# Kernel optimization log

Measured on AMD Instinct MI355X. Metric: run time of the kernel, lower is better.

Reference implementation:

```python
import jax, jax.numpy as jnp
import numpy as np

P_DROP = 0.1

def setup_inputs() -> dict:
    key = jax.random.key(0)
    kq, kk, kv, km = jax.random.split(key, 4)
    B, H, S, D = 2, 16, 2048, 128
    q = jax.random.normal(kq, (B, H, S, D), dtype=jnp.float32)
    k = jax.random.normal(kk, (B, H, S, D), dtype=jnp.float32)
    v = jax.random.normal(kv, (B, H, S, D), dtype=jnp.float32)
    # Deterministic inverted-dropout mask: keep with prob 1-p, scaled by 1/(1-p)
    keep = jax.random.bernoulli(km, 1.0 - P_DROP, (B, H, S, S))
    drop_mask = keep.astype(jnp.float32) / jnp.float32(1.0 - P_DROP)
    return {"q": q, "k": k, "v": v, "drop_mask": drop_mask}

def reference(q, k, v, drop_mask):
    # qk: [B,H,S,S] = q @ k^T (no softmax, per the original module)
    qk = jnp.einsum("bhsd,bhtd->bhst", q, k)
    dropped = qk * drop_mask  # inverted dropout, p=0.1
    out = jnp.einsum("bhst,bhtd->bhsd", dropped, v)
    return out
```

## Files before the change

kernel.cpp:

```cpp
#include <hip/hip_runtime.h>

#define S_LEN 2048
#define D_DIM 128
#define BM 128
#define BK 64
#define NIT (S_LEN / BK)
#define LQ 136
#define LV 72

typedef __attribute__((ext_vector_type(8))) short bf16x8;
typedef __attribute__((ext_vector_type(4))) float f32x4;
typedef __attribute__((ext_vector_type(4))) int i32x4;

__device__ __forceinline__ unsigned short f2bf(float x) {
    union { float f; unsigned u; } c; c.f = x;
    unsigned r = c.u + 0x7fffu + ((c.u >> 16) & 1u);
    return (unsigned short)(r >> 16);
}
__device__ __forceinline__ unsigned pack2(float a, float b) {
    return (unsigned)f2bf(a) | ((unsigned)f2bf(b) << 16);
}

__global__ __launch_bounds__(256, 2)
void fused_qkmv(const float* __restrict__ q, const float* __restrict__ k,
                const float* __restrict__ v, const float* __restrict__ mask,
                float* __restrict__ out) {
    __shared__ unsigned short Qs[BM * LQ];
    __shared__ unsigned short Ks[BK * LQ];
    __shared__ unsigned short Vt[D_DIM * LV];

    const int tid  = threadIdx.x;
    const int lane = tid & 63;
    const int w    = tid >> 6;
    const int l15  = lane & 15;
    const int qd   = lane >> 4;

    const int bh = blockIdx.x >> 4;
    const int s0 = (blockIdx.x & 15) * BM;

    const float* qp = q + (size_t)bh * S_LEN * D_DIM;
    const float* kp = k + (size_t)bh * S_LEN * D_DIM;
    const float* vp = v + (size_t)bh * S_LEN * D_DIM;
    const float* mp = mask + (size_t)bh * S_LEN * S_LEN;
    float*       op = out + (size_t)bh * S_LEN * D_DIM;

    {
        const int r = tid >> 5, d = (tid & 31) * 4;
#pragma unroll
        for (int sw = 0; sw < 16; ++sw) {
            const int row = sw * 8 + r;
            float4 f = *(const float4*)(qp + (size_t)(s0 + row) * D_DIM + d);
            uint2 wv; wv.x = pack2(f.x, f.y); wv.y = pack2(f.z, f.w);
            *(uint2*)&Qs[row * LQ + d] = wv;
        }
    }

    f32x4 acc_o[2][8];
#pragma unroll
    for (int i = 0; i < 2; ++i)
#pragma unroll
        for (int j = 0; j < 8; ++j) acc_o[i][j] = (f32x4){0.f, 0.f, 0.f, 0.f};

    const int a0 = ((2 * (qd & 1)) * 16 + l15) * 4;
    const int a1 = a0 + 64;
    const bool hi = (qd >= 2);

    for (int it = 0; it < NIT; ++it) {
        const int t0 = it * BK;

        float4 mreg[4][2];
        {
            const float* mb = mp + (size_t)(s0 + 32 * w + l15) * S_LEN + t0 + 4 * qd;
#pragma unroll
            for (int ti = 0; ti < 4; ++ti)
#pragma unroll
                for (int sj = 0; sj < 2; ++sj)
                    mreg[ti][sj] = *(const float4*)(mb + (size_t)sj * 16 * S_LEN + ti * 16);
        }

        {
            const int tk = tid >> 2, dk = (tid & 3) * 4;
            float4 f[8];
#pragma unroll
            for (int i = 0; i < 8; ++i)
                f[i] = *(const float4*)(kp + (size_t)(t0 + tk) * D_DIM + dk + 16 * i);
#pragma unroll
            for (int i = 0; i < 8; ++i) {
                uint2 wv; wv.x = pack2(f[i].x, f[i].y); wv.y = pack2(f[i].z, f[i].w);
                *(uint2*)&Ks[tk * LQ + dk + 16 * i] = wv;
            }
        }
        {
            const int tg = (tid & 15) * 4, dg = (tid >> 4) * 8;
            float4 ra[4], rb[4];
#pragma unroll
            for (int r = 0; r < 4; ++r) {
                ra[r] = *(const float4*)(vp + (size_t)(t0 + tg + r) * D_DIM + dg);
                rb[r] = *(const float4*)(vp + (size_t)(t0 + tg + r) * D_DIM + dg + 4);
            }
#pragma unroll
            for (int i = 0; i < 4; ++i) {
                uint2 wv;
                wv.x = pack2(((const float*)&ra[0])[i], ((const float*)&ra[1])[i]);
                wv.y = pack2(((const float*)&ra[2])[i], ((const float*)&ra[3])[i]);
                *(uint2*)&Vt[(dg + i) * LV + tg] = wv;
                uint2 wv2;
                wv2.x = pack2(((const float*)&rb[0])[i], ((const float*)&rb[1])[i]);
                wv2.y = pack2(((const float*)&rb[2])[i], ((const float*)&rb[3])[i]);
                *(uint2*)&Vt[(dg + 4 + i) * LV + tg] = wv2;
            }
        }

        f32x4 acc_s[4][2];
#pragma unroll
        for (int i = 0; i < 4; ++i)
#pragma unroll
            for (int j = 0; j < 2; ++j) acc_s[i][j] = (f32x4){0.f, 0.f, 0.f, 0.f};

        __syncthreads();

#pragma unroll
        for (int kc = 0; kc < 4; ++kc) {
            const int ko = kc * 32 + qd * 8;
            bf16x8 af[4], bq[2];
#pragma unroll
            for (int ti = 0; ti < 4; ++ti)
                af[ti] = *(const bf16x8*)&Ks[(16 * ti + l15) * LQ + ko];
#pragma unroll
            for (int sj = 0; sj < 2; ++sj)
                bq[sj] = *(const bf16x8*)&Qs[(32 * w + 16 * sj + l15) * LQ + ko];
#pragma unroll
            for (int ti = 0; ti < 4; ++ti)
#pragma unroll
                for (int sj = 0; sj < 2; ++sj)
                    acc_s[ti][sj] = __builtin_amdgcn_mfma_f32_16x16x32_bf16(
                        af[ti], bq[sj], acc_s[ti][sj], 0, 0, 0);
        }

        int pu[4][2][2];
#pragma unroll
        for (int ti = 0; ti < 4; ++ti)
#pragma unroll
            for (int sj = 0; sj < 2; ++sj) {
                f32x4 sv = acc_s[ti][sj];
                float4 m = mreg[ti][sj];
                pu[ti][sj][0] = (int)pack2(sv[0] * m.x, sv[1] * m.y);
                pu[ti][sj][1] = (int)pack2(sv[2] * m.z, sv[3] * m.w);
            }

#pragma unroll
        for (int kc2 = 0; kc2 < 2; ++kc2) {
            bf16x8 ap[2];
#pragma unroll
            for (int sj = 0; sj < 2; ++sj) {
                const int tA = 2 * kc2, tB = 2 * kc2 + 1;
                int w0a = __builtin_amdgcn_ds_bpermute(a0, pu[tA][sj][0]);
                int w0b = __builtin_amdgcn_ds_bpermute(a0, pu[tB][sj][0]);
                int w1a = __builtin_amdgcn_ds_bpermute(a0, pu[tA][sj][1]);
                int w1b = __builtin_amdgcn_ds_bpermute(a0, pu[tB][sj][1]);
                int w2a = __builtin_amdgcn_ds_bpermute(a1, pu[tA][sj][0]);
                int w2b = __builtin_amdgcn_ds_bpermute(a1, pu[tB][sj][0]);
                int w3a = __builtin_amdgcn_ds_bpermute(a1, pu[tA][sj][1]);
                int w3b = __builtin_amdgcn_ds_bpermute(a1, pu[tB][sj][1]);
                union { i32x4 i; bf16x8 b; } u;
                u.i = (i32x4){hi ? w0b : w0a, hi ? w1b : w1a,
                              hi ? w2b : w2a, hi ? w3b : w3a};
                ap[sj] = u.b;
            }
            const int ko = kc2 * 32 + qd * 8;
#pragma unroll
            for (int dj = 0; dj < 8; ++dj) {
                bf16x8 bv = *(const bf16x8*)&Vt[(16 * dj + l15) * LV + ko];
#pragma unroll
                for (int si = 0; si < 2; ++si)
                    acc_o[si][dj] = __builtin_amdgcn_mfma_f32_16x16x32_bf16(
                        ap[si], bv, acc_o[si][dj], 0, 0, 0);
            }
        }

        __syncthreads();
    }

#pragma unroll
    for (int si = 0; si < 2; ++si)
#pragma unroll
        for (int dj = 0; dj < 8; ++dj) {
#pragma unroll
            for (int r = 0; r < 4; ++r) {
                const int srow = s0 + 32 * w + 16 * si + 4 * qd + r;
                op[(size_t)srow * D_DIM + 16 * dj + l15] = acc_o[si][dj][r];
            }
        }
}

extern "C" void kernel_launch(void* const* d_in, const int* in_sizes, int n_in,
                              void* d_out, int out_size, void* d_ws, size_t ws_size,
                              hipStream_t stream) {
    const float* q = (const float*)d_in[0];
    const float* k = (const float*)d_in[1];
    const float* v = (const float*)d_in[2];
    const float* m = (const float*)d_in[3];
    float* out = (float*)d_out;
    fused_qkmv<<<dim3(512), dim3(256), 0, stream>>>(q, k, v, m, out);
}
```

Baseline: 794.5 us.

## Double-buffer K/V tiles with register prefetch and keep Q fragments in registers

Converts the main loop into a software pipeline. The next K, V and mask tiles are loaded from global memory into registers while the current tile's MFMAs run, then written into a second LDS buffer, so each iteration needs one barrier instead of two. Q fragments are loaded once into registers, which removes the per-iteration Q LDS reads. The bf16 conversion also changes from round-to-nearest-even to a cheaper round-half-up using v_perm, which adds register pressure and slightly changes rounding.

```diff
diff --git a/kernel.cpp b/kernel.cpp
--- a/kernel.cpp
+++ b/kernel.cpp
@@ -7,27 +7,28 @@
 #define NIT (S_LEN / BK)
 #define LQ 136
 #define LV 72
+#define KS_E (BK * LQ)
+#define VT_E (D_DIM * LV)
+#define BUF_E (KS_E + VT_E)
 
 typedef __attribute__((ext_vector_type(8))) short bf16x8;
 typedef __attribute__((ext_vector_type(4))) float f32x4;
 typedef __attribute__((ext_vector_type(4))) int i32x4;
 
-__device__ __forceinline__ unsigned short f2bf(float x) {
+__device__ __forceinline__ unsigned rnd16(float x) {
     union { float f; unsigned u; } c; c.f = x;
-    unsigned r = c.u + 0x7fffu + ((c.u >> 16) & 1u);
-    return (unsigned short)(r >> 16);
-}
-__device__ __forceinline__ unsigned pack2(float a, float b) {
-    return (unsigned)f2bf(a) | ((unsigned)f2bf(b) << 16);
+    return c.u + 0x8000u;
+}
+__device__ __forceinline__ unsigned pack2(float lo, float hi) {
+    return __builtin_amdgcn_perm(rnd16(hi), rnd16(lo), 0x07060302);
 }
 
 __global__ __launch_bounds__(256, 2)
 void fused_qkmv(const float* __restrict__ q, const float* __restrict__ k,
                 const float* __restrict__ v, const float* __restrict__ mask,
                 float* __restrict__ out) {
-    __shared__ unsigned short Qs[BM * LQ];
-    __shared__ unsigned short Ks[BK * LQ];
-    __shared__ unsigned short Vt[D_DIM * LV];
+    __shared__ __align__(16) unsigned short smem[2 * BUF_E];
+    unsigned short* const Qst = smem;
 
     const int tid  = threadIdx.x;
     const int lane = tid & 63;
@@ -44,16 +45,60 @@
     const float* mp = mask + (size_t)bh * S_LEN * S_LEN;
     float*       op = out + (size_t)bh * S_LEN * D_DIM;
 
+    const int rr = tid >> 5, dd = (tid & 31) * 4;
+    const int tg = (tid & 15) * 4, dg = (tid >> 4) * 8;
+
+    float4 kf[8];
+#pragma unroll
+    for (int sw = 0; sw < 8; ++sw)
+        kf[sw] = *(const float4*)(kp + (size_t)(sw * 8 + rr) * D_DIM + dd);
+    float4 va[4], vb[4];
+#pragma unroll
+    for (int r = 0; r < 4; ++r) {
+        va[r] = *(const float4*)(vp + (size_t)(tg + r) * D_DIM + dg);
+        vb[r] = *(const float4*)(vp + (size_t)(tg + r) * D_DIM + dg + 4);
+    }
+    float4 mreg[4][2];
     {
-        const int r = tid >> 5, d = (tid & 31) * 4;
-#pragma unroll
-        for (int sw = 0; sw < 16; ++sw) {
-            const int row = sw * 8 + r;
-            float4 f = *(const float4*)(qp + (size_t)(s0 + row) * D_DIM + d);
-            uint2 wv; wv.x = pack2(f.x, f.y); wv.y = pack2(f.z, f.w);
-            *(uint2*)&Qs[row * LQ + d] = wv;
-        }
-    }
+        const float* mb = mp + (size_t)(s0 + 32 * w + l15) * S_LEN + 4 * qd;
+#pragma unroll
+        for (int ti = 0; ti < 4; ++ti)
+#pragma unroll
+            for (int sj = 0; sj < 2; ++sj)
+                mreg[ti][sj] = *(const float4*)(mb + (size_t)sj * 16 * S_LEN + ti * 16);
+    }
+#pragma unroll
+    for (int sw = 0; sw < 16; ++sw) {
+        const int row = sw * 8 + rr;
+        float4 f = *(const float4*)(qp + (size_t)(s0 + row) * D_DIM + dd);
+        uint2 wv; wv.x = pack2(f.x, f.y); wv.y = pack2(f.z, f.w);
+        *(uint2*)&Qst[row * LQ + dd] = wv;
+    }
+    __syncthreads();
+    bf16x8 qf[2][4];
+#pragma unroll
+    for (int sj = 0; sj < 2; ++sj)
+#pragma unroll
+        for (int kc = 0; kc < 4; ++kc)
+            qf[sj][kc] = *(const bf16x8*)&Qst[(32 * w + 16 * sj + l15) * LQ + kc * 32 + qd * 8];
+    __syncthreads();
+#pragma unroll
+    for (int sw = 0; sw < 8; ++sw) {
+        uint2 wv; wv.x = pack2(kf[sw].x, kf[sw].y); wv.y = pack2(kf[sw].z, kf[sw].w);
+        *(uint2*)&smem[(sw * 8 + rr) * LQ + dd] = wv;
+    }
+#pragma unroll
+    for (int i = 0; i < 4; ++i) {
+        uint2 wv;
+        wv.x = pack2(((const float*)&va[0])[i], ((const float*)&va[1])[i]);
+        wv.y = pack2(((const float*)&va[2])[i], ((const float*)&va[3])[i]);
+        *(uint2*)&smem[KS_E + (dg + i) * LV + tg] = wv;
+        uint2 wv2;
+        wv2.x = pack2(((const float*)&vb[0])[i], ((const float*)&vb[1])[i]);
+        wv2.y = pack2(((const float*)&vb[2])[i], ((const float*)&vb[3])[i]);
+        *(uint2*)&smem[KS_E + (dg + 4 + i) * LV + tg] = wv2;
+    }
+    __syncthreads();
 
     f32x4 acc_o[2][8];
 #pragma unroll
@@ -65,50 +110,20 @@
     const int a1 = a0 + 64;
     const bool hi = (qd >= 2);
 
+    int cur = 0;
     for (int it = 0; it < NIT; ++it) {
-        const int t0 = it * BK;
-
-        float4 mreg[4][2];
-        {
-            const float* mb = mp + (size_t)(s0 + 32 * w + l15) * S_LEN + t0 + 4 * qd;
-#pragma unroll
-            for (int ti = 0; ti < 4; ++ti)
-#pragma unroll
-                for (int sj = 0; sj < 2; ++sj)
-                    mreg[ti][sj] = *(const float4*)(mb + (size_t)sj * 16 * S_LEN + ti * 16);
-        }
-
-        {
-            const int tk = tid >> 2, dk = (tid & 3) * 4;
-            float4 f[8];
-#pragma unroll
-            for (int i = 0; i < 8; ++i)
-                f[i] = *(const float4*)(kp + (size_t)(t0 + tk) * D_DIM + dk + 16 * i);
-#pragma unroll
-            for (int i = 0; i < 8; ++i) {
-                uint2 wv; wv.x = pack2(f[i].x, f[i].y); wv.y = pack2(f[i].z, f[i].w);
-                *(uint2*)&Ks[tk * LQ + dk + 16 * i] = wv;
-            }
-        }
-        {
-            const int tg = (tid & 15) * 4, dg = (tid >> 4) * 8;
-            float4 ra[4], rb[4];
-#pragma unroll
-            for (int r = 0; r < 4; ++r) {
-                ra[r] = *(const float4*)(vp + (size_t)(t0 + tg + r) * D_DIM + dg);
-                rb[r] = *(const float4*)(vp + (size_t)(t0 + tg + r) * D_DIM + dg + 4);
-            }
-#pragma unroll
-            for (int i = 0; i < 4; ++i) {
-                uint2 wv;
-                wv.x = pack2(((const float*)&ra[0])[i], ((const float*)&ra[1])[i]);
-                wv.y = pack2(((const float*)&ra[2])[i], ((const float*)&ra[3])[i]);
-                *(uint2*)&Vt[(dg + i) * LV + tg] = wv;
-                uint2 wv2;
-                wv2.x = pack2(((const float*)&rb[0])[i], ((const float*)&rb[1])[i]);
-                wv2.y = pack2(((const float*)&rb[2])[i], ((const float*)&rb[3])[i]);
-                *(uint2*)&Vt[(dg + 4 + i) * LV + tg] = wv2;
-            }
+        const int nxt = cur ^ 1;
+        const int tn = (it + 1) * BK;
+        const bool pf = (it + 1 < NIT);
+        const unsigned short* Ksc = smem + cur * BUF_E;
+        const unsigned short* Vtc = smem + cur * BUF_E + KS_E;
+        unsigned short* Ksn = smem + nxt * BUF_E;
+        unsigned short* Vtn = smem + nxt * BUF_E + KS_E;
+
+        if (pf) {
+#pragma unroll
+            for (int sw = 0; sw < 8; ++sw)
+                kf[sw] = *(const float4*)(kp + (size_t)(tn + sw * 8 + rr) * D_DIM + dd);
         }
 
         f32x4 acc_s[4][2];
@@ -116,25 +131,32 @@
         for (int i = 0; i < 4; ++i)
 #pragma unroll
             for (int j = 0; j < 2; ++j) acc_s[i][j] = (f32x4){0.f, 0.f, 0.f, 0.f};
-
-        __syncthreads();
-
 #pragma unroll
         for (int kc = 0; kc < 4; ++kc) {
             const int ko = kc * 32 + qd * 8;
-            bf16x8 af[4], bq[2];
+            bf16x8 af[4];
 #pragma unroll
             for (int ti = 0; ti < 4; ++ti)
-                af[ti] = *(const bf16x8*)&Ks[(16 * ti + l15) * LQ + ko];
-#pragma unroll
-            for (int sj = 0; sj < 2; ++sj)
-                bq[sj] = *(const bf16x8*)&Qs[(32 * w + 16 * sj + l15) * LQ + ko];
+                af[ti] = *(const bf16x8*)&Ksc[(16 * ti + l15) * LQ + ko];
 #pragma unroll
             for (int ti = 0; ti < 4; ++ti)
 #pragma unroll
                 for (int sj = 0; sj < 2; ++sj)
                     acc_s[ti][sj] = __builtin_amdgcn_mfma_f32_16x16x32_bf16(
-                        af[ti], bq[sj], acc_s[ti][sj], 0, 0, 0);
+                        af[ti], qf[sj][kc], acc_s[ti][sj], 0, 0, 0);
+        }
+
+        if (pf) {
+#pragma unroll
+            for (int sw = 0; sw < 8; ++sw) {
+                uint2 wv; wv.x = pack2(kf[sw].x, kf[sw].y); wv.y = pack2(kf[sw].z, kf[sw].w);
+                *(uint2*)&Ksn[(sw * 8 + rr) * LQ + dd] = wv;
+            }
+#pragma unroll
+            for (int r = 0; r < 4; ++r) {
+                va[r] = *(const float4*)(vp + (size_t)(tn + tg + r) * D_DIM + dg);
+                vb[r] = *(const float4*)(vp + (size_t)(tn + tg + r) * D_DIM + dg + 4);
+            }
         }
 
         int pu[4][2][2];
@@ -147,6 +169,15 @@
                 pu[ti][sj][0] = (int)pack2(sv[0] * m.x, sv[1] * m.y);
                 pu[ti][sj][1] = (int)pack2(sv[2] * m.z, sv[3] * m.w);
             }
+
+        if (pf) {
+            const float* mb = mp + (size_t)(s0 + 32 * w + l15) * S_LEN + tn + 4 * qd;
+#pragma unroll
+            for (int ti = 0; ti < 4; ++ti)
+#pragma unroll
+                for (int sj = 0; sj < 2; ++sj)
+                    mreg[ti][sj] = *(const float4*)(mb + (size_t)sj * 16 * S_LEN + ti * 16);
+        }
 
 #pragma unroll
         for (int kc2 = 0; kc2 < 2; ++kc2) {
@@ -170,7 +201,7 @@
             const int ko = kc2 * 32 + qd * 8;
 #pragma unroll
             for (int dj = 0; dj < 8; ++dj) {
-                bf16x8 bv = *(const bf16x8*)&Vt[(16 * dj + l15) * LV + ko];
+                bf16x8 bv = *(const bf16x8*)&Vtc[(16 * dj + l15) * LV + ko];
 #pragma unroll
                 for (int si = 0; si < 2; ++si)
                     acc_o[si][dj] = __builtin_amdgcn_mfma_f32_16x16x32_bf16(
@@ -178,7 +209,22 @@
             }
         }
 
+        if (pf) {
+#pragma unroll
+            for (int i = 0; i < 4; ++i) {
+                uint2 wv;
+                wv.x = pack2(((const float*)&va[0])[i], ((const float*)&va[1])[i]);
+                wv.y = pack2(((const float*)&va[2])[i], ((const float*)&va[3])[i]);
+                *(uint2*)&Vtn[(dg + i) * LV + tg] = wv;
+                uint2 wv2;
+                wv2.x = pack2(((const float*)&vb[0])[i], ((const float*)&vb[1])[i]);
+                wv2.y = pack2(((const float*)&vb[2])[i], ((const float*)&vb[3])[i]);
+                *(uint2*)&Vtn[(dg + 4 + i) * LV + tg] = wv2;
+            }
+        }
+
         __syncthreads();
+        cur = nxt;
     }
 
 #pragma unroll
```

New measurement: 807.7 us. Within noise of the previous version (+1.7%).

## Use 8 waves per block with register-held Q fragments and V prefetch

Applied to the files above, without the earlier changes.

Doubles the block to 512 threads so each wave owns 16 query rows instead of 32. Q is converted once into shared memory, then held in registers as MFMA fragments, which frees LDS for only K and transposed V. The next tile's V is prefetched into registers while the current tile is computed, and the mask loads are issued after the barrier. The bf16 packing switches to a cheaper round-half-up plus byte-permute. This aims to raise occupancy and hide global latency, at the cost of more per-thread K loads and slightly different rounding.

```diff
diff --git a/kernel.cpp b/kernel.cpp
--- a/kernel.cpp
+++ b/kernel.cpp
@@ -7,27 +7,26 @@
 #define NIT (S_LEN / BK)
 #define LQ 136
 #define LV 72
+#define KS_E (BK * LQ)
+#define VT_E (D_DIM * LV)
 
 typedef __attribute__((ext_vector_type(8))) short bf16x8;
 typedef __attribute__((ext_vector_type(4))) float f32x4;
 typedef __attribute__((ext_vector_type(4))) int i32x4;
 
-__device__ __forceinline__ unsigned short f2bf(float x) {
+__device__ __forceinline__ unsigned rnd16(float x) {
     union { float f; unsigned u; } c; c.f = x;
-    unsigned r = c.u + 0x7fffu + ((c.u >> 16) & 1u);
-    return (unsigned short)(r >> 16);
+    return c.u + 0x8000u;
 }
-__device__ __forceinline__ unsigned pack2(float a, float b) {
-    return (unsigned)f2bf(a) | ((unsigned)f2bf(b) << 16);
+__device__ __forceinline__ unsigned pack2(float lo, float hi) {
+    return __builtin_amdgcn_perm(rnd16(hi), rnd16(lo), 0x07060302);
 }
 
-__global__ __launch_bounds__(256, 2)
+__global__ __launch_bounds__(512, 4)
 void fused_qkmv(const float* __restrict__ q, const float* __restrict__ k,
                 const float* __restrict__ v, const float* __restrict__ mask,
                 float* __restrict__ out) {
-    __shared__ unsigned short Qs[BM * LQ];
-    __shared__ unsigned short Ks[BK * LQ];
-    __shared__ unsigned short Vt[D_DIM * LV];
+    __shared__ __align__(16) unsigned short smem[KS_E + VT_E];
 
     const int tid  = threadIdx.x;
     const int lane = tid & 63;
@@ -44,22 +43,43 @@
     const float* mp = mask + (size_t)bh * S_LEN * S_LEN;
     float*       op = out + (size_t)bh * S_LEN * D_DIM;
 
-    {
-        const int r = tid >> 5, d = (tid & 31) * 4;
+    const int kr  = tid >> 3;
+    const int kc0 = (tid & 7) * 16;
+    const int tg  = (tid & 15) * 4;
+    const int dg  = (tid >> 4) * 4;
+
+    float4 vf[4];
 #pragma unroll
-        for (int sw = 0; sw < 16; ++sw) {
-            const int row = sw * 8 + r;
-            float4 f = *(const float4*)(qp + (size_t)(s0 + row) * D_DIM + d);
-            uint2 wv; wv.x = pack2(f.x, f.y); wv.y = pack2(f.z, f.w);
-            *(uint2*)&Qs[row * LQ + d] = wv;
-        }
+    for (int r = 0; r < 4; ++r)
+        vf[r] = *(const float4*)(vp + (size_t)(tg + r) * D_DIM + dg);
+
+#pragma unroll
+    for (int p = 0; p < 2; ++p) {
+        const int row = 64 * p + kr;
+        float4 f0 = *(const float4*)(qp + (size_t)(s0 + row) * D_DIM + kc0);
+        float4 f1 = *(const float4*)(qp + (size_t)(s0 + row) * D_DIM + kc0 + 4);
+        float4 f2 = *(const float4*)(qp + (size_t)(s0 + row) * D_DIM + kc0 + 8);
+        float4 f3 = *(const float4*)(qp + (size_t)(s0 + row) * D_DIM + kc0 + 12);
+        uint2 wv;
+        wv.x = pack2(f0.x, f0.y); wv.y = pack2(f0.z, f0.w);
+        *(uint2*)&smem[row * LQ + kc0] = wv;
+        wv.x = pack2(f1.x, f1.y); wv.y = pack2(f1.z, f1.w);
+        *(uint2*)&smem[row * LQ + kc0 + 4] = wv;
+        wv.x = pack2(f2.x, f2.y); wv.y = pack2(f2.z, f2.w);
+        *(uint2*)&smem[row * LQ + kc0 + 8] = wv;
+        wv.x = pack2(f3.x, f3.y); wv.y = pack2(f3.z, f3.w);
+        *(uint2*)&smem[row * LQ + kc0 + 12] = wv;
     }
+    __syncthreads();
+    bf16x8 qf[4];
+#pragma unroll
+    for (int kc = 0; kc < 4; ++kc)
+        qf[kc] = *(const bf16x8*)&smem[(16 * w + l15) * LQ + kc * 32 + qd * 8];
+    __syncthreads();
 
-    f32x4 acc_o[2][8];
+    f32x4 acc_o[8];
 #pragma unroll
-    for (int i = 0; i < 2; ++i)
-#pragma unroll
-        for (int j = 0; j < 8; ++j) acc_o[i][j] = (f32x4){0.f, 0.f, 0.f, 0.f};
+    for (int j = 0; j < 8; ++j) acc_o[j] = (f32x4){0.f, 0.f, 0.f, 0.f};
 
     const int a0 = ((2 * (qd & 1)) * 16 + l15) * 4;
     const int a1 = a0 + 64;
@@ -68,113 +88,90 @@
     for (int it = 0; it < NIT; ++it) {
         const int t0 = it * BK;
 
-        float4 mreg[4][2];
+        float4 kf0 = *(const float4*)(kp + (size_t)(t0 + kr) * D_DIM + kc0);
+        float4 kf1 = *(const float4*)(kp + (size_t)(t0 + kr) * D_DIM + kc0 + 4);
+        float4 kf2 = *(const float4*)(kp + (size_t)(t0 + kr) * D_DIM + kc0 + 8);
+        float4 kf3 = *(const float4*)(kp + (size_t)(t0 + kr) * D_DIM + kc0 + 12);
+#pragma unroll
+        for (int i = 0; i < 4; ++i) {
+            uint2 wv;
+            wv.x = pack2(((const float*)&vf[0])[i], ((const float*)&vf[1])[i]);
+            wv.y = pack2(((const float*)&vf[2])[i], ((const float*)&vf[3])[i]);
+            *(uint2*)&smem[KS_E + (dg + i) * LV + tg] = wv;
+        }
         {
-            const float* mb = mp + (size_t)(s0 + 32 * w + l15) * S_LEN + t0 + 4 * qd;
+            uint2 wv;
+            wv.x = pack2(kf0.x, kf0.y); wv.y = pack2(kf0.z, kf0.w);
+            *(uint2*)&smem[kr * LQ + kc0] = wv;
+            wv.x = pack2(kf1.x, kf1.y); wv.y = pack2(kf1.z, kf1.w);
+            *(uint2*)&smem[kr * LQ + kc0 + 4] = wv;
+            wv.x = pack2(kf2.x, kf2.y); wv.y = pack2(kf2.z, kf2.w);
+            *(uint2*)&smem[kr * LQ + kc0 + 8] = wv;
+            wv.x = pack2(kf3.x, kf3.y); wv.y = pack2(kf3.z, kf3.w);
+            *(uint2*)&smem[kr * LQ + kc0 + 12] = wv;
+        }
+        __syncthreads();
+
+        float4 mreg[4];
+        {
+            const float* mb = mp + (size_t)(s0 + 16 * w + l15) * S_LEN + t0 + 4 * qd;
 #pragma unroll
             for (int ti = 0; ti < 4; ++ti)
-#pragma unroll
-                for (int sj = 0; sj < 2; ++sj)
-                    mreg[ti][sj] = *(const float4*)(mb + (size_t)sj * 16 * S_LEN + ti * 16);
+                mreg[ti] = *(const float4*)(mb + ti * 16);
         }
 
-        {
-            const int tk = tid >> 2, dk = (tid & 3) * 4;
-            float4 f[8];
+        f32x4 acc_s[4];
 #pragma unroll
-            for (int i = 0; i < 8; ++i)
-                f[i] = *(const float4*)(kp + (size_t)(t0 + tk) * D_DIM + dk + 16 * i);
-#pragma unroll
-            for (int i = 0; i < 8; ++i) {
-                uint2 wv; wv.x = pack2(f[i].x, f[i].y); wv.y = pack2(f[i].z, f[i].w);
-                *(uint2*)&Ks[tk * LQ + dk + 16 * i] = wv;
-            }
-        }
-        {
-            const int tg = (tid & 15) * 4, dg = (tid >> 4) * 8;
-            float4 ra[4], rb[4];
-#pragma unroll
-            for (int r = 0; r < 4; ++r) {
-                ra[r] = *(const float4*)(vp + (size_t)(t0 + tg + r) * D_DIM + dg);
-                rb[r] = *(const float4*)(vp + (size_t)(t0 + tg + r) * D_DIM + dg + 4);
-            }
-#pragma unroll
-            for (int i = 0; i < 4; ++i) {
-                uint2 wv;
-                wv.x = pack2(((const float*)&ra[0])[i], ((const float*)&ra[1])[i]);
-                wv.y = pack2(((const float*)&ra[2])[i], ((const float*)&ra[3])[i]);
-                *(uint2*)&Vt[(dg + i) * LV + tg] = wv;
-                uint2 wv2;
-                wv2.x = pack2(((const float*)&rb[0])[i], ((const float*)&rb[1])[i]);
-                wv2.y = pack2(((const float*)&rb[2])[i], ((const float*)&rb[3])[i]);
-                *(uint2*)&Vt[(dg + 4 + i) * LV + tg] = wv2;
-            }
-        }
-
-        f32x4 acc_s[4][2];
-#pragma unroll
-        for (int i = 0; i < 4; ++i)
-#pragma unroll
-            for (int j = 0; j < 2; ++j) acc_s[i][j] = (f32x4){0.f, 0.f, 0.f, 0.f};
-
-        __syncthreads();
-
+        for (int i = 0; i < 4; ++i) acc_s[i] = (f32x4){0.f, 0.f, 0.f, 0.f};
 #pragma unroll
         for (int kc = 0; kc < 4; ++kc) {
             const int ko = kc * 32 + qd * 8;
-            bf16x8 af[4], bq[2];
+            bf16x8 af[4];
 #pragma unroll
             for (int ti = 0; ti < 4; ++ti)
-                af[ti] = *(const bf16x8*)&Ks[(16 * ti + l15) * LQ + ko];
-#pragma unroll
-            for (int sj = 0; sj < 2; ++sj)
-                bq[sj] = *(const bf16x8*)&Qs[(32 * w + 16 * sj + l15) * LQ + ko];
+                af[ti] = *(const bf16x8*)&smem[(16 * ti + l15) * LQ + ko];
 #pragma unroll
             for (int ti = 0; ti < 4; ++ti)
-#pragma unroll
-                for (int sj = 0; sj < 2; ++sj)
-                    acc_s[ti][sj] = __builtin_amdgcn_mfma_f32_16x16x32_bf16(
-                        af[ti], bq[sj], acc_s[ti][sj], 0, 0, 0);
+                acc_s[ti] = __builtin_amdgcn_mfma_f32_16x16x32_bf16(
+                    af[ti], qf[kc], acc_s[ti], 0, 0, 0);
         }
 
-        int pu[4][2][2];
+        if (it + 1 < NIT) {
+            const int tn = t0 + BK;
 #pragma unroll
-        for (int ti = 0; ti < 4; ++ti)
+            for (int r = 0; r < 4; ++r)
+                vf[r] = *(const float4*)(vp + (size_t)(tn + tg + r) * D_DIM + dg);
+        }
+
+        int pu[4][2];
 #pragma unroll
-            for (int sj = 0; sj < 2; ++sj) {
-                f32x4 sv = acc_s[ti][sj];
-                float4 m = mreg[ti][sj];
-                pu[ti][sj][0] = (int)pack2(sv[0] * m.x, sv[1] * m.y);
-                pu[ti][sj][1] = (int)pack2(sv[2] * m.z, sv[3] * m.w);
-            }
+        for (int ti = 0; ti < 4; ++ti) {
+            f32x4 sv = acc_s[ti];
+            float4 m = mreg[ti];
+            pu[ti][0] = (int)pack2(sv[0] * m.x, sv[1] * m.y);
+            pu[ti][1] = (int)pack2(sv[2] * m.z, sv[3] * m.w);
+        }
 
 #pragma unroll
         for (int kc2 = 0; kc2 < 2; ++kc2) {
-            bf16x8 ap[2];
-#pragma unroll
-            for (int sj = 0; sj < 2; ++sj) {
-                const int tA = 2 * kc2, tB = 2 * kc2 + 1;
-                int w0a = __builtin_amdgcn_ds_bpermute(a0, pu[tA][sj][0]);
-                int w0b = __builtin_amdgcn_ds_bpermute(a0, pu[tB][sj][0]);
-                int w1a = __builtin_amdgcn_ds_bpermute(a0, pu[tA][sj][1]);
-                int w1b = __builtin_amdgcn_ds_bpermute(a0, pu[tB][sj][1]);
-                int w2a = __builtin_amdgcn_ds_bpermute(a1, pu[tA][sj][0]);
-                int w2b = __builtin_amdgcn_ds_bpermute(a1, pu[tB][sj][0]);
-                int w3a = __builtin_amdgcn_ds_bpermute(a1, pu[tA][sj][1]);
-                int w3b = __builtin_amdgcn_ds_bpermute(a1, pu[tB][sj][1]);
-                union { i32x4 i; bf16x8 b; } u;
-                u.i = (i32x4){hi ? w0b : w0a, hi ? w1b : w1a,
-                              hi ? w2b : w2a, hi ? w3b : w3a};
-                ap[sj] = u.b;
-            }
+            const int tA = 2 * kc2, tB = 2 * kc2 + 1;
+            int w0a = __builtin_amdgcn_ds_bpermute(a0, pu[tA][0]);
+            int w0b = __builtin_amdgcn_ds_bpermute(a0, pu[tB][0]);
+            int w1a = __builtin_amdgcn_ds_bpermute(a0, pu[tA][1]);
+            int w1b = __builtin_amdgcn_ds_bpermute(a0, pu[tB][1]);
+            int w2a = __builtin_amdgcn_ds_bpermute(a1, pu[tA][0]);
+            int w2b = __builtin_amdgcn_ds_bpermute(a1, pu[tB][0]);
+            int w3a = __builtin_amdgcn_ds_bpermute(a1, pu[tA][1]);
+            int w3b = __builtin_amdgcn_ds_bpermute(a1, pu[tB][1]);
+            union { i32x4 i; bf16x8 b; } u;
+            u.i = (i32x4){hi ? w0b : w0a, hi ? w1b : w1a,
+                          hi ? w2b : w2a, hi ? w3b : w3a};
             const int ko = kc2 * 32 + qd * 8;
 #pragma unroll
             for (int dj = 0; dj < 8; ++dj) {
-                bf16x8 bv = *(const bf16x8*)&Vt[(16 * dj + l15) * LV + ko];
-#pragma unroll
-                for (int si = 0; si < 2; ++si)
-                    acc_o[si][dj] = __builtin_amdgcn_mfma_f32_16x16x32_bf16(
-                        ap[si], bv, acc_o[si][dj], 0, 0, 0);
+                bf16x8 bv = *(const bf16x8*)&smem[KS_E + (16 * dj + l15) * LV + ko];
+                acc_o[dj] = __builtin_amdgcn_mfma_f32_16x16x32_bf16(
+                    u.b, bv, acc_o[dj], 0, 0, 0);
             }
         }
 
@@ -182,14 +179,11 @@
     }
 
 #pragma unroll
-    for (int si = 0; si < 2; ++si)
+    for (int dj = 0; dj < 8; ++dj)
 #pragma unroll
-        for (int dj = 0; dj < 8; ++dj) {
-#pragma unroll
-            for (int r = 0; r < 4; ++r) {
-                const int srow = s0 + 32 * w + 16 * si + 4 * qd + r;
-                op[(size_t)srow * D_DIM + 16 * dj + l15] = acc_o[si][dj][r];
-            }
+        for (int r = 0; r < 4; ++r) {
+            const int srow = s0 + 16 * w + 4 * qd + r;
+            op[(size_t)srow * D_DIM + 16 * dj + l15] = acc_o[dj][r];
         }
 }
 
@@ -201,5 +195,5 @@
     const float* v = (const float*)d_in[2];
     const float* m = (const float*)d_in[3];
     float* out = (float*)d_out;
-    fused_qkmv<<<dim3(512), dim3(256), 0, stream>>>(q, k, v, m, out);
+    fused_qkmv<<<dim3(512), dim3(512), 0, stream>>>(q, k, v, m, out);
 }
```

Measured after the change: 869.3 us. +9.4%, slower.
